# Optimization experiments

Hardware: AMD Instinct MI355X
Metric: run time of the kernel (lower is better)

The kernel has to match this reference:

```python
import jax, jax.numpy as jnp
import numpy as np

N = 20000      # nodes per snapshot
E = 320000     # directed edges per snapshot (self-loops added in reference)
T = 8          # snapshot sequence length
IN = 1         # in_dim
H = 32         # hidden_dim
HEADS = 2      # heads in first GAT layer
EPS = 1e-16    # PyG softmax denominator epsilon


def setup_inputs() -> dict:
    key = jax.random.key(0)
    ks = jax.random.split(key, 20)
    s = 0.1  # weight scale for numerical sanity
    return {
        "x": jax.random.normal(ks[0], (T, N, IN), jnp.float32),
        "edge_index": jax.random.randint(ks[1], (T, 2, E), 0, N, jnp.int64),
        # GAT layer 1: in=1 -> heads=2, out=32 (concat -> 64)
        "W1": jax.random.normal(ks[2], (IN, HEADS * H), jnp.float32) * s,
        "att_src1": jax.random.normal(ks[3], (HEADS, H), jnp.float32) * s,
        "att_dst1": jax.random.normal(ks[4], (HEADS, H), jnp.float32) * s,
        "b1": jax.random.normal(ks[5], (HEADS * H,), jnp.float32) * s,
        # GAT layer 2: in=64 -> heads=1, out=32
        "W2": jax.random.normal(ks[6], (HEADS * H, H), jnp.float32) * s,
        "att_src2": jax.random.normal(ks[7], (1, H), jnp.float32) * s,
        "att_dst2": jax.random.normal(ks[8], (1, H), jnp.float32) * s,
        "b2": jax.random.normal(ks[9], (H,), jnp.float32) * s,
        # GRU (torch layout: rows ordered r,z,n)
        "gru_w_ih": jax.random.normal(ks[10], (3 * H, H), jnp.float32) * s,
        "gru_w_hh": jax.random.normal(ks[11], (3 * H, H), jnp.float32) * s,
        "gru_b_ih": jax.random.normal(ks[12], (3 * H,), jnp.float32) * s,
        "gru_b_hh": jax.random.normal(ks[13], (3 * H,), jnp.float32) * s,
        # output head
        "fc_w": jax.random.normal(ks[14], (1, H), jnp.float32) * s,
        "fc_b": jax.random.normal(ks[15], (1,), jnp.float32) * s,
    }


def _gat_layer(x, src, dst, W, att_src, att_dst, bias, heads, dh):
    """PyG GATConv (shared src/dst lin, leaky_relu 0.2, per-dest softmax, concat heads)."""
    h = (x @ W).reshape(N, heads, dh)                      # [N,Hd,D]
    a_src = jnp.sum(h * att_src, axis=-1)                  # [N,Hd]
    a_dst = jnp.sum(h * att_dst, axis=-1)                  # [N,Hd]
    e = jax.nn.leaky_relu(a_src[src] + a_dst[dst], 0.2)    # [Eh,Hd]
    m = jax.ops.segment_max(e, dst, num_segments=N)        # per-dest max (stable)
    ex = jnp.exp(e - m[dst])
    denom = jax.ops.segment_sum(ex, dst, num_segments=N)
    alpha = ex / (denom[dst] + EPS)                        # [Eh,Hd]
    msg = h[src] * alpha[..., None]                        # [Eh,Hd,D]
    out = jax.ops.segment_sum(msg, dst, num_segments=N)    # [N,Hd,D]
    return out.reshape(N, heads * dh) + bias


def _encode(x_t, ei_t, W1, att_src1, att_dst1, b1, W2, att_src2, att_dst2, b2):
    loops = jnp.arange(N, dtype=ei_t.dtype)                # GATConv add_self_loops=True
    src = jnp.concatenate([ei_t[0], loops])
    dst = jnp.concatenate([ei_t[1], loops])
    h = jax.nn.elu(_gat_layer(x_t, src, dst, W1, att_src1, att_dst1, b1, HEADS, H))
    h = jax.nn.elu(_gat_layer(h, src, dst, W2, att_src2, att_dst2, b2, 1, H))
    return h                                                # [N,H]


def reference(x, edge_index, W1, att_src1, att_dst1, b1, W2, att_src2, att_dst2, b2,
              gru_w_ih, gru_w_hh, gru_b_ih, gru_b_hh, fc_w, fc_b):
    enc = jax.vmap(lambda xt, et: _encode(xt, et, W1, att_src1, att_dst1, b1,
                                          W2, att_src2, att_dst2, b2))(x, edge_index)  # [T,N,H]

    def gru_step(h, x_t):
        gi = x_t @ gru_w_ih.T + gru_b_ih                   # [N,3H]
        gh = h @ gru_w_hh.T + gru_b_hh
        ir, iz, in_ = jnp.split(gi, 3, axis=-1)
        hr, hz, hn = jnp.split(gh, 3, axis=-1)
        r = jax.nn.sigmoid(ir + hr)
        z = jax.nn.sigmoid(iz + hz)
        n = jnp.tanh(in_ + r * hn)
        h_new = (1.0 - z) * n + z * h
        return h_new, None

    h0 = jnp.zeros((N, H), enc.dtype)
    h_last, _ = jax.lax.scan(gru_step, h0, enc)            # last timestep hidden [N,H]
    pred = h_last @ fc_w.T + fc_b                          # [N,1]
    return pred
```

## Files before the change

kernel.cpp:

```cpp
#include <hip/hip_runtime.h>
#include <cmath>

#define NN 20000
#define NE 320000
#define TT 8
#define EPSF 1e-16f
#define NR 32
#define RSZ 625
#define NCH 1250

#define OFF_RT  0
#define OFF_ROW 1024
#define OFF_CSR (OFF_ROW + TT*(NN+1))
#define OFF_H2S (OFF_CSR + TT*NE/2)
#define OFF_AS2 (OFF_H2S + TT*NN*32)
#define OFF_AD2 (OFF_AS2 + TT*NN)
#define OFF_ENC (OFF_AD2 + TT*NN)
#define OFF_WP  (OFF_ENC + TT*NN*32)
#define WS_WORDS (OFF_WP + 6144)

__device__ __forceinline__ float fexp(float x) { return __expf(x); }
__device__ __forceinline__ float fsigmoid(float x) { return 1.f / (1.f + __expf(-x)); }
__device__ __forceinline__ float ftanh(float x) {
    float ax = fabsf(x);
    float e2 = __expf(-2.f * ax);
    float th = (1.f - e2) / (1.f + e2);
    return copysignf(th, x);
}

__global__ __launch_bounds__(256) void k_bhist(const int* __restrict__ ei,
                                               int* __restrict__ bh,
                                               const float* __restrict__ wih,
                                               const float* __restrict__ whh,
                                               float* __restrict__ wp) {
    int b = blockIdx.x;
    int t = b & 7, c = b >> 3;
    __shared__ int cnt[NR];
    int tid = threadIdx.x;
    if (b < 4) {
        int i = b * 256 + tid;
        int k = i >> 5, j = i & 31;
        ((float4*)wp)[i] = make_float4(wih[j * 32 + k], wih[(32 + j) * 32 + k],
                                       wih[(64 + j) * 32 + k], whh[j * 32 + k]);
        ((float2*)(wp + 4096))[i] = make_float2(whh[(32 + j) * 32 + k],
                                                whh[(64 + j) * 32 + k]);
    }
    if (tid < NR) cnt[tid] = 0;
    __syncthreads();
    int e = c * 256 + tid;
    int dst = ei[(size_t)t * 2 * NE + NE + e];
    int r = dst / RSZ;
    atomicAdd(&cnt[r], 1);
    __syncthreads();
    if (tid < NR) bh[(t * NCH + c) * NR + tid] = cnt[tid];
}

__global__ __launch_bounds__(256) void k_bscan1(int* __restrict__ bh,
                                                int* __restrict__ rt) {
    int b = blockIdx.x;
    int t = b & 7, r = b >> 3;
    __shared__ int sums[256];
    int tid = threadIdx.x;
    int c0 = tid * 5, c1 = c0 + 5; if (c1 > NCH) c1 = NCH; if (c0 > NCH) c0 = NCH;
    int v[5]; int s = 0;
    for (int c = c0, k = 0; c < c1; c++, k++) { v[k] = bh[(t * NCH + c) * NR + r]; s += v[k]; }
    sums[tid] = s;
    __syncthreads();
    if (tid == 0) {
        int acc = 0;
        for (int i = 0; i < 256; i++) { int x = sums[i]; sums[i] = acc; acc += x; }
        rt[t * NR + r] = acc;
    }
    __syncthreads();
    int acc = sums[tid];
    for (int c = c0, k = 0; c < c1; c++, k++) { bh[(t * NCH + c) * NR + r] = acc; acc += v[k]; }
}

__global__ __launch_bounds__(256) void k_bplace(const int* __restrict__ ei,
                                                const int* __restrict__ bh,
                                                const int* __restrict__ rt,
                                                unsigned* __restrict__ bkt) {
    int b = blockIdx.x;
    int t = b & 7, c = b >> 3;
    __shared__ int cnt[NR], base[NR], rbs[NR];
    int tid = threadIdx.x;
    if (tid == 0) {
        int acc = 0;
        for (int r = 0; r < NR; r++) { rbs[r] = acc; acc += rt[t * NR + r]; }
    }
    if (tid < NR) {
        cnt[tid] = 0;
        base[tid] = bh[(t * NCH + c) * NR + tid];
    }
    __syncthreads();
    int e = c * 256 + tid;
    int src = ei[(size_t)t * 2 * NE + e];
    int dst = ei[(size_t)t * 2 * NE + NE + e];
    int r = dst / RSZ;
    int pos = atomicAdd(&cnt[r], 1);
    bkt[(size_t)t * NE + rbs[r] + base[r] + pos] =
        ((unsigned)src << 10) | (unsigned)(dst - r * RSZ);
}

__global__ __launch_bounds__(256) void k_csr(const unsigned* __restrict__ bkt,
                                             const int* __restrict__ rt,
                                             int* __restrict__ row,
                                             unsigned short* __restrict__ csr) {
    int b = blockIdx.x;
    int t = b & 7, r = b >> 3;
    __shared__ int segs[2];
    __shared__ int deg[RSZ];
    __shared__ int cur[RSZ];
    __shared__ int sums[256];
    int tid = threadIdx.x;
    if (tid == 0) {
        int acc = 0, s0 = 0;
        for (int i = 0; i < NR; i++) { if (i == r) s0 = acc; acc += rt[t * NR + i]; }
        segs[0] = s0;
        segs[1] = (r == NR - 1) ? acc : s0 + rt[t * NR + r];
    }
    for (int i = tid; i < RSZ; i += 256) deg[i] = 0;
    __syncthreads();
    int seg0 = segs[0], seg1 = segs[1];
    int lo = r * RSZ;
    const unsigned* bp = bkt + (size_t)t * NE;
    for (int i = seg0 + tid; i < seg1; i += 256)
        atomicAdd(&deg[bp[i] & 1023], 1);
    __syncthreads();
    int c0 = tid * 3, c1 = c0 + 3; if (c1 > RSZ) c1 = RSZ; if (c0 > RSZ) c0 = RSZ;
    int v[3]; int s = 0;
    for (int i = c0, k = 0; i < c1; i++, k++) { v[k] = deg[i]; s += v[k]; }
    sums[tid] = s;
    __syncthreads();
    if (tid == 0) {
        int acc = 0;
        for (int i = 0; i < 256; i++) { int x = sums[i]; sums[i] = acc; acc += x; }
    }
    __syncthreads();
    int acc = sums[tid];
    for (int i = c0, k = 0; i < c1; i++, k++) {
        int off = seg0 + acc;
        row[t * (NN + 1) + lo + i] = off;
        cur[i] = off;
        acc += v[k];
    }
    if (r == NR - 1 && tid == 0) row[t * (NN + 1) + NN] = seg1;
    __syncthreads();
    unsigned short* cp = csr + (size_t)t * NE;
    for (int i = seg0 + tid; i < seg1; i += 256) {
        unsigned pk = bp[i];
        int pos = atomicAdd(&cur[pk & 1023], 1);
        cp[pos] = (unsigned short)(pk >> 10);
    }
}

__global__ __launch_bounds__(256) void k_l1(
        const float* __restrict__ x, const int* __restrict__ row,
        const unsigned short* __restrict__ csr,
        const float* __restrict__ as1, const float* __restrict__ ad1,
        const float* __restrict__ W1, const float* __restrict__ b1,
        const float* __restrict__ W2,
        const float* __restrict__ as2w, const float* __restrict__ ad2w,
        float* __restrict__ h2s, float* __restrict__ as2, float* __restrict__ ad2) {
    __shared__ float sW2[64 * 32];
    __shared__ float sW1[64], sb1[64], sas[32], sad[32], sc[4];
    int tid = threadIdx.x;
    for (int i = tid; i < 64 * 32; i += 256) sW2[i] = W2[i];
    if (tid < 64) { sW1[tid] = W1[tid]; sb1[tid] = b1[tid]; }
    if (tid < 32) { sas[tid] = as2w[tid]; sad[tid] = ad2w[tid]; }
    if (tid < 4) {
        int hd = tid & 1;
        const float* att = (tid < 2) ? as1 : ad1;
        float s = 0.f;
        for (int k = 0; k < 32; k++) s += W1[hd * 32 + k] * att[hd * 32 + k];
        sc[tid] = s;
    }
    __syncthreads();
    int b = blockIdx.x;
    int t = b & 7, chunk = b >> 3;
    int n = chunk * 256 + tid;
    if (n >= NN) return;
    int idx = t * NN + n;
    float cs0 = sc[0], cs1 = sc[1], cd0 = sc[2], cd1 = sc[3];
    float xd = x[idx];
    float v0 = xd * (cs0 + cd0); v0 = v0 > 0.f ? v0 : 0.2f * v0; float ex0 = fexp(v0);
    float v1 = xd * (cs1 + cd1); v1 = v1 > 0.f ? v1 : 0.2f * v1; float ex1 = fexp(v1);
    float den0 = ex0, den1 = ex1, S0 = ex0 * xd, S1 = ex1 * xd;
    int rs = row[t * (NN + 1) + n], re = row[t * (NN + 1) + n + 1];
    const unsigned short* cp = csr + (size_t)t * NE;
    const float* xp = x + t * NN;
    int i = rs;
    for (; i < re && (i & 3); i++) {
        int src = cp[i];
        float xs = xp[src];
        float u0 = xs * cs0 + xd * cd0; u0 = u0 > 0.f ? u0 : 0.2f * u0; float q0 = fexp(u0);
        float u1 = xs * cs1 + xd * cd1; u1 = u1 > 0.f ? u1 : 0.2f * u1; float q1 = fexp(u1);
        den0 += q0; S0 += q0 * xs;
        den1 += q1; S1 += q1 * xs;
    }
    for (; i + 4 <= re; i += 4) {
        ushort4 s4 = *(const ushort4*)(cp + i);
        float xA = xp[s4.x], xB = xp[s4.y], xC = xp[s4.z], xD = xp[s4.w];
        float uA0 = xA * cs0 + xd * cd0; uA0 = uA0 > 0.f ? uA0 : 0.2f * uA0; float qA0 = fexp(uA0);
        float uB0 = xB * cs0 + xd * cd0; uB0 = uB0 > 0.f ? uB0 : 0.2f * uB0; float qB0 = fexp(uB0);
        float uC0 = xC * cs0 + xd * cd0; uC0 = uC0 > 0.f ? uC0 : 0.2f * uC0; float qC0 = fexp(uC0);
        float uD0 = xD * cs0 + xd * cd0; uD0 = uD0 > 0.f ? uD0 : 0.2f * uD0; float qD0 = fexp(uD0);
        float uA1 = xA * cs1 + xd * cd1; uA1 = uA1 > 0.f ? uA1 : 0.2f * uA1; float qA1 = fexp(uA1);
        float uB1 = xB * cs1 + xd * cd1; uB1 = uB1 > 0.f ? uB1 : 0.2f * uB1; float qB1 = fexp(uB1);
        float uC1 = xC * cs1 + xd * cd1; uC1 = uC1 > 0.f ? uC1 : 0.2f * uC1; float qC1 = fexp(uC1);
        float uD1 = xD * cs1 + xd * cd1; uD1 = uD1 > 0.f ? uD1 : 0.2f * uD1; float qD1 = fexp(uD1);
        den0 += (qA0 + qB0) + (qC0 + qD0);
        S0 += qA0 * xA + qB0 * xB + qC0 * xC + qD0 * xD;
        den1 += (qA1 + qB1) + (qC1 + qD1);
        S1 += qA1 * xA + qB1 * xB + qC1 * xC + qD1 * xD;
    }
    for (; i < re; i++) {
        int src = cp[i];
        float xs = xp[src];
        float u0 = xs * cs0 + xd * cd0; u0 = u0 > 0.f ? u0 : 0.2f * u0; float q0 = fexp(u0);
        float u1 = xs * cs1 + xd * cd1; u1 = u1 > 0.f ? u1 : 0.2f * u1; float q1 = fexp(u1);
        den0 += q0; S0 += q0 * xs;
        den1 += q1; S1 += q1 * xs;
    }
    S0 /= (den0 + EPSF);
    S1 /= (den1 + EPSF);
    float h1[64];
#pragma unroll
    for (int d = 0; d < 64; d++) {
        float v = sW1[d] * (d < 32 ? S0 : S1) + sb1[d];
        h1[d] = v > 0.f ? v : fexp(v) - 1.f;
    }
    float a_s = 0.f, a_d = 0.f;
    float acc[32];
#pragma unroll 4
    for (int j = 0; j < 32; j++) {
        float a = 0.f;
#pragma unroll
        for (int d = 0; d < 64; d++) a += h1[d] * sW2[d * 32 + j];
        acc[j] = a;
        a_s += a * sas[j];
        a_d += a * sad[j];
    }
    float4* op = (float4*)(h2s + (size_t)idx * 32);
#pragma unroll
    for (int q = 0; q < 8; q++)
        op[q] = make_float4(acc[4 * q], acc[4 * q + 1], acc[4 * q + 2], acc[4 * q + 3]);
    as2[idx] = a_s;
    ad2[idx] = a_d;
}

__global__ __launch_bounds__(256) void k_l2(
        const int* __restrict__ row, const unsigned short* __restrict__ csr,
        const float* __restrict__ as2, const float* __restrict__ ad2,
        const float* __restrict__ h2s, const float* __restrict__ b2,
        float* __restrict__ enc) {
    __shared__ float2 qoff[8][32];
    int tid = threadIdx.x;
    int g = tid >> 5, lane = tid & 31;
    int b = blockIdx.x;
    int t = b & 7, chunk = b >> 3;
    int n = chunk * 8 + g;
    int pair = t * NN + n;
    int base = t * NN;
    const float* hb = h2s + (size_t)base * 32;
    float adn = ad2[pair];
    float vs = as2[pair] + adn; vs = vs > 0.f ? vs : 0.2f * vs;
    float qs = fexp(vs);
    float num = qs * hb[(size_t)n * 32 + lane];
    float den_part = 0.f;
    int rs = row[t * (NN + 1) + n], re = row[t * (NN + 1) + n + 1];
    const unsigned short* cp = csr + (size_t)t * NE;
    for (int i0 = rs; i0 < re; i0 += 32) {
        int cnt = re - i0; if (cnt > 32) cnt = 32;
        float q = 0.f;
        if (lane < cnt) {
            int s = cp[i0 + lane];
            float a = as2[base + s];
            float u = a + adn; u = u > 0.f ? u : 0.2f * u;
            q = fexp(u);
            qoff[g][lane] = make_float2(q, __int_as_float(s * 32));
        }
        den_part += q;
        __builtin_amdgcn_wave_barrier();
        int e = 0;
        for (; e + 4 <= cnt; e += 4) {
            float4 p0 = *(const float4*)&qoff[g][e];
            float4 p1 = *(const float4*)&qoff[g][e + 2];
            num += p0.x * hb[__float_as_int(p0.y) + lane];
            num += p0.z * hb[__float_as_int(p0.w) + lane];
            num += p1.x * hb[__float_as_int(p1.y) + lane];
            num += p1.z * hb[__float_as_int(p1.w) + lane];
        }
        for (; e + 2 <= cnt; e += 2) {
            float4 p0 = *(const float4*)&qoff[g][e];
            num += p0.x * hb[__float_as_int(p0.y) + lane];
            num += p0.z * hb[__float_as_int(p0.w) + lane];
        }
        if (e < cnt) {
            float2 p = qoff[g][e];
            num += p.x * hb[__float_as_int(p.y) + lane];
        }
        __builtin_amdgcn_wave_barrier();
    }
    float den = den_part;
#pragma unroll
    for (int off = 16; off > 0; off >>= 1) den += __shfl_xor(den, off, 32);
    den += qs;
    float ev = num / (den + EPSF) + b2[lane];
    ev = ev > 0.f ? ev : fexp(ev) - 1.f;
    enc[(size_t)pair * 32 + lane] = ev;
}

__global__ __launch_bounds__(128) void k_gru(
        const float* __restrict__ enc, const float* __restrict__ wp,
        const float* __restrict__ bih, const float* __restrict__ bhh,
        const float* __restrict__ fcw, const float* __restrict__ fcb,
        float* __restrict__ out) {
    __shared__ float4 wpA[32 * 32];
    __shared__ float2 wpB[32 * 32];
    __shared__ float sbih[96], sbhh[96], sfw[32];
    __shared__ float4 e4[4][32], h4[4][32];
    int tid = threadIdx.x;
    const float4* wpAg = (const float4*)wp;
    const float2* wpBg = (const float2*)(wp + 4096);
    for (int i = tid; i < 1024; i += 128) { wpA[i] = wpAg[i]; wpB[i] = wpBg[i]; }
    if (tid < 96) { sbih[tid] = bih[tid]; sbhh[tid] = bhh[tid]; }
    if (tid < 32) sfw[tid] = fcw[tid];
    int g = tid >> 5, lane = tid & 31;
    int n0 = blockIdx.x * 16 + g * 4;
    float h0 = 0.f, h1 = 0.f, h2 = 0.f, h3 = 0.f;
    h4[g][lane] = make_float4(0.f, 0.f, 0.f, 0.f);
    __syncthreads();
    float bi_r = sbih[lane], bi_z = sbih[32 + lane], bi_n = sbih[64 + lane];
    float bh_r = sbhh[lane], bh_z = sbhh[32 + lane], bh_n = sbhh[64 + lane];
    const float* ep0 = enc + (size_t)n0 * 32 + lane;
    float4 ecur = make_float4(ep0[0], ep0[32], ep0[64], ep0[96]);
    for (int t = 0; t < TT; t++) {
        e4[g][lane] = ecur;
        __builtin_amdgcn_wave_barrier();
        if (t < TT - 1) {
            const float* ep = enc + ((size_t)((t + 1) * NN + n0)) * 32 + lane;
            ecur = make_float4(ep[0], ep[32], ep[64], ep[96]);
        }
        float ir0 = bi_r, ir1 = bi_r, ir2 = bi_r, ir3 = bi_r;
        float iz0 = bi_z, iz1 = bi_z, iz2 = bi_z, iz3 = bi_z;
        float in0 = bi_n, in1 = bi_n, in2 = bi_n, in3 = bi_n;
        float hr0 = bh_r, hr1 = bh_r, hr2 = bh_r, hr3 = bh_r;
        float hz0 = bh_z, hz1 = bh_z, hz2 = bh_z, hz3 = bh_z;
        float hn0 = bh_n, hn1 = bh_n, hn2 = bh_n, hn3 = bh_n;
#pragma unroll 16
        for (int k = 0; k < 32; k++) {
            float4 wa = wpA[k * 32 + lane];
            float2 wb = wpB[k * 32 + lane];
            float4 ek = e4[g][k];
            float4 hk = h4[g][k];
            ir0 += wa.x * ek.x; ir1 += wa.x * ek.y; ir2 += wa.x * ek.z; ir3 += wa.x * ek.w;
            iz0 += wa.y * ek.x; iz1 += wa.y * ek.y; iz2 += wa.y * ek.z; iz3 += wa.y * ek.w;
            in0 += wa.z * ek.x; in1 += wa.z * ek.y; in2 += wa.z * ek.z; in3 += wa.z * ek.w;
            hr0 += wa.w * hk.x; hr1 += wa.w * hk.y; hr2 += wa.w * hk.z; hr3 += wa.w * hk.w;
            hz0 += wb.x * hk.x; hz1 += wb.x * hk.y; hz2 += wb.x * hk.z; hz3 += wb.x * hk.w;
            hn0 += wb.y * hk.x; hn1 += wb.y * hk.y; hn2 += wb.y * hk.z; hn3 += wb.y * hk.w;
        }
        __builtin_amdgcn_wave_barrier();
        {
            float r, z, nn_;
            r = fsigmoid(ir0 + hr0); z = fsigmoid(iz0 + hz0);
            nn_ = ftanh(in0 + r * hn0); h0 = (1.f - z) * nn_ + z * h0;
            r = fsigmoid(ir1 + hr1); z = fsigmoid(iz1 + hz1);
            nn_ = ftanh(in1 + r * hn1); h1 = (1.f - z) * nn_ + z * h1;
            r = fsigmoid(ir2 + hr2); z = fsigmoid(iz2 + hz2);
            nn_ = ftanh(in2 + r * hn2); h2 = (1.f - z) * nn_ + z * h2;
            r = fsigmoid(ir3 + hr3); z = fsigmoid(iz3 + hz3);
            nn_ = ftanh(in3 + r * hn3); h3 = (1.f - z) * nn_ + z * h3;
        }
        h4[g][lane] = make_float4(h0, h1, h2, h3);
        __builtin_amdgcn_wave_barrier();
    }
    float fw = sfw[lane], fb = fcb[0];
    float v0 = h0 * fw, v1 = h1 * fw, v2 = h2 * fw, v3 = h3 * fw;
#pragma unroll
    for (int off = 16; off > 0; off >>= 1) {
        v0 += __shfl_down(v0, off, 32);
        v1 += __shfl_down(v1, off, 32);
        v2 += __shfl_down(v2, off, 32);
        v3 += __shfl_down(v3, off, 32);
    }
    if (lane == 0) {
        out[n0 + 0] = v0 + fb;
        out[n0 + 1] = v1 + fb;
        out[n0 + 2] = v2 + fb;
        out[n0 + 3] = v3 + fb;
    }
}

extern "C" void kernel_launch(void* const* d_in, const int* in_sizes, int n_in,
                              void* d_out, int out_size, void* d_ws, size_t ws_size,
                              hipStream_t stream) {
    const float* x    = (const float*)d_in[0];
    const int*   ei   = (const int*)d_in[1];
    const float* W1   = (const float*)d_in[2];
    const float* as1  = (const float*)d_in[3];
    const float* ad1  = (const float*)d_in[4];
    const float* b1   = (const float*)d_in[5];
    const float* W2   = (const float*)d_in[6];
    const float* as2w = (const float*)d_in[7];
    const float* ad2w = (const float*)d_in[8];
    const float* b2   = (const float*)d_in[9];
    const float* wih  = (const float*)d_in[10];
    const float* whh  = (const float*)d_in[11];
    const float* bih  = (const float*)d_in[12];
    const float* bhh  = (const float*)d_in[13];
    const float* fcw  = (const float*)d_in[14];
    const float* fcb  = (const float*)d_in[15];
    float* ws  = (float*)d_ws;
    float* out = (float*)d_out;

    int*            rt   = (int*)(ws + OFF_RT);
    int*            rowp = (int*)(ws + OFF_ROW);
    unsigned short* csr  = (unsigned short*)(ws + OFF_CSR);
    int*            bh   = (int*)(ws + OFF_H2S);
    unsigned*       bkt  = (unsigned*)(ws + OFF_ENC);
    float*          wp   = ws + OFF_WP;

    k_bhist<<<TT * NCH, 256, 0, stream>>>(ei, bh, wih, whh, wp);
    k_bscan1<<<TT * NR, 256, 0, stream>>>(bh, rt);
    k_bplace<<<TT * NCH, 256, 0, stream>>>(ei, bh, rt, bkt);
    k_csr<<<TT * NR, 256, 0, stream>>>(bkt, rt, rowp, csr);

    k_l1<<<TT * ((NN + 255) / 256), 256, 0, stream>>>(x, rowp, csr, as1, ad1,
                                              W1, b1, W2, as2w, ad2w,
                                              ws + OFF_H2S, ws + OFF_AS2, ws + OFF_AD2);

    k_l2<<<TT * (NN / 8), 256, 0, stream>>>(rowp, csr, ws + OFF_AS2, ws + OFF_AD2,
                                            ws + OFF_H2S, b2, ws + OFF_ENC);

    k_gru<<<NN / 16, 128, 0, stream>>>(ws + OFF_ENC, wp, bih, bhh,
                                       fcw, fcb, out);
}
```

Measured before the change: 256.4 us.

## Precompute GRU input projections for all timesteps before recurrent loop

The GRU kernel now computes the input-gate projections for all 8 timesteps in a first loop, keeping them in registers (48 floats per thread), then runs the recurrence with only the hidden-state matvec on the serial path. Each wave handles 2 nodes instead of 4 with 256-thread blocks, and the packed weight layout is split into separate input and hidden arrays. This shortens the dependent chain per step and adds waves, at the cost of higher register pressure from the stored projections.

```diff
diff --git a/kernel.cpp b/kernel.cpp
--- a/kernel.cpp
+++ b/kernel.cpp
@@ -40,10 +40,10 @@
     if (b < 4) {
         int i = b * 256 + tid;
         int k = i >> 5, j = i & 31;
-        ((float4*)wp)[i] = make_float4(wih[j * 32 + k], wih[(32 + j) * 32 + k],
-                                       wih[(64 + j) * 32 + k], whh[j * 32 + k]);
-        ((float2*)(wp + 4096))[i] = make_float2(whh[(32 + j) * 32 + k],
-                                                whh[(64 + j) * 32 + k]);
+        ((float2*)wp)[i] = make_float2(wih[j * 32 + k], wih[(32 + j) * 32 + k]);
+        wp[2048 + i] = wih[(64 + j) * 32 + k];
+        ((float2*)(wp + 3072))[i] = make_float2(whh[j * 32 + k], whh[(32 + j) * 32 + k]);
+        wp[5120 + i] = whh[(64 + j) * 32 + k];
     }
     if (tid < NR) cnt[tid] = 0;
     __syncthreads();
@@ -311,85 +311,94 @@
     enc[(size_t)pair * 32 + lane] = ev;
 }
 
-__global__ __launch_bounds__(128) void k_gru(
+__global__ __launch_bounds__(256) void k_gru(
         const float* __restrict__ enc, const float* __restrict__ wp,
         const float* __restrict__ bih, const float* __restrict__ bhh,
         const float* __restrict__ fcw, const float* __restrict__ fcb,
         float* __restrict__ out) {
-    __shared__ float4 wpA[32 * 32];
-    __shared__ float2 wpB[32 * 32];
+    __shared__ float2 wIa[1024];
+    __shared__ float  wIb[1024];
+    __shared__ float2 wHa[1024];
+    __shared__ float  wHb[1024];
     __shared__ float sbih[96], sbhh[96], sfw[32];
-    __shared__ float4 e4[4][32], h4[4][32];
-    int tid = threadIdx.x;
-    const float4* wpAg = (const float4*)wp;
-    const float2* wpBg = (const float2*)(wp + 4096);
-    for (int i = tid; i < 1024; i += 128) { wpA[i] = wpAg[i]; wpB[i] = wpBg[i]; }
+    __shared__ float2 ebuf[8][32], hbuf[8][32];
+    int tid = threadIdx.x;
+    for (int i = tid; i < 1024; i += 256) {
+        wIa[i] = ((const float2*)wp)[i];
+        wIb[i] = wp[2048 + i];
+        wHa[i] = ((const float2*)(wp + 3072))[i];
+        wHb[i] = wp[5120 + i];
+    }
     if (tid < 96) { sbih[tid] = bih[tid]; sbhh[tid] = bhh[tid]; }
     if (tid < 32) sfw[tid] = fcw[tid];
     int g = tid >> 5, lane = tid & 31;
-    int n0 = blockIdx.x * 16 + g * 4;
-    float h0 = 0.f, h1 = 0.f, h2 = 0.f, h3 = 0.f;
-    h4[g][lane] = make_float4(0.f, 0.f, 0.f, 0.f);
-    __syncthreads();
+    int n0 = blockIdx.x * 16 + g * 2;
+    float h0 = 0.f, h1 = 0.f;
+    hbuf[g][lane] = make_float2(0.f, 0.f);
+    __syncthreads();
+    float gi[TT][6];
+#pragma unroll
+    for (int t = 0; t < TT; t++)
+#pragma unroll
+        for (int q = 0; q < 6; q++) gi[t][q] = 0.f;
+    const float* ebase = enc + (size_t)n0 * 32 + lane;
+    float e0 = ebase[0], e1 = ebase[32];
+#pragma unroll
+    for (int t = 0; t < TT; t++) {
+        ebuf[g][lane] = make_float2(e0, e1);
+        __builtin_amdgcn_wave_barrier();
+        if (t < TT - 1) {
+            const float* ep = ebase + (size_t)(t + 1) * NN * 32;
+            e0 = ep[0]; e1 = ep[32];
+        }
+#pragma unroll
+        for (int k = 0; k < 32; k++) {
+            float2 wa = wIa[k * 32 + lane];
+            float  wn = wIb[k * 32 + lane];
+            float2 ek = ebuf[g][k];
+            gi[t][0] += wa.x * ek.x; gi[t][1] += wa.x * ek.y;
+            gi[t][2] += wa.y * ek.x; gi[t][3] += wa.y * ek.y;
+            gi[t][4] += wn   * ek.x; gi[t][5] += wn   * ek.y;
+        }
+        __builtin_amdgcn_wave_barrier();
+    }
     float bi_r = sbih[lane], bi_z = sbih[32 + lane], bi_n = sbih[64 + lane];
     float bh_r = sbhh[lane], bh_z = sbhh[32 + lane], bh_n = sbhh[64 + lane];
-    const float* ep0 = enc + (size_t)n0 * 32 + lane;
-    float4 ecur = make_float4(ep0[0], ep0[32], ep0[64], ep0[96]);
+#pragma unroll
     for (int t = 0; t < TT; t++) {
-        e4[g][lane] = ecur;
-        __builtin_amdgcn_wave_barrier();
-        if (t < TT - 1) {
-            const float* ep = enc + ((size_t)((t + 1) * NN + n0)) * 32 + lane;
-            ecur = make_float4(ep[0], ep[32], ep[64], ep[96]);
-        }
-        float ir0 = bi_r, ir1 = bi_r, ir2 = bi_r, ir3 = bi_r;
-        float iz0 = bi_z, iz1 = bi_z, iz2 = bi_z, iz3 = bi_z;
-        float in0 = bi_n, in1 = bi_n, in2 = bi_n, in3 = bi_n;
-        float hr0 = bh_r, hr1 = bh_r, hr2 = bh_r, hr3 = bh_r;
-        float hz0 = bh_z, hz1 = bh_z, hz2 = bh_z, hz3 = bh_z;
-        float hn0 = bh_n, hn1 = bh_n, hn2 = bh_n, hn3 = bh_n;
-#pragma unroll 16
+        float hr0 = bh_r, hr1 = bh_r, hz0 = bh_z, hz1 = bh_z;
+        float hn0 = bh_n, hn1 = bh_n;
+#pragma unroll
         for (int k = 0; k < 32; k++) {
-            float4 wa = wpA[k * 32 + lane];
-            float2 wb = wpB[k * 32 + lane];
-            float4 ek = e4[g][k];
-            float4 hk = h4[g][k];
-            ir0 += wa.x * ek.x; ir1 += wa.x * ek.y; ir2 += wa.x * ek.z; ir3 += wa.x * ek.w;
-            iz0 += wa.y * ek.x; iz1 += wa.y * ek.y; iz2 += wa.y * ek.z; iz3 += wa.y * ek.w;
-            in0 += wa.z * ek.x; in1 += wa.z * ek.y; in2 += wa.z * ek.z; in3 += wa.z * ek.w;
-            hr0 += wa.w * hk.x; hr1 += wa.w * hk.y; hr2 += wa.w * hk.z; hr3 += wa.w * hk.w;
-            hz0 += wb.x * hk.x; hz1 += wb.x * hk.y; hz2 += wb.x * hk.z; hz3 += wb.x * hk.w;
-            hn0 += wb.y * hk.x; hn1 += wb.y * hk.y; hn2 += wb.y * hk.z; hn3 += wb.y * hk.w;
-        }
-        __builtin_amdgcn_wave_barrier();
-        {
-            float r, z, nn_;
-            r = fsigmoid(ir0 + hr0); z = fsigmoid(iz0 + hz0);
-            nn_ = ftanh(in0 + r * hn0); h0 = (1.f - z) * nn_ + z * h0;
-            r = fsigmoid(ir1 + hr1); z = fsigmoid(iz1 + hz1);
-            nn_ = ftanh(in1 + r * hn1); h1 = (1.f - z) * nn_ + z * h1;
-            r = fsigmoid(ir2 + hr2); z = fsigmoid(iz2 + hz2);
-            nn_ = ftanh(in2 + r * hn2); h2 = (1.f - z) * nn_ + z * h2;
-            r = fsigmoid(ir3 + hr3); z = fsigmoid(iz3 + hz3);
-            nn_ = ftanh(in3 + r * hn3); h3 = (1.f - z) * nn_ + z * h3;
-        }
-        h4[g][lane] = make_float4(h0, h1, h2, h3);
+            float2 wa = wHa[k * 32 + lane];
+            float  wn = wHb[k * 32 + lane];
+            float2 hk = hbuf[g][k];
+            hr0 += wa.x * hk.x; hr1 += wa.x * hk.y;
+            hz0 += wa.y * hk.x; hz1 += wa.y * hk.y;
+            hn0 += wn   * hk.x; hn1 += wn   * hk.y;
+        }
+        __builtin_amdgcn_wave_barrier();
+        float r0 = fsigmoid(gi[t][0] + bi_r + hr0);
+        float r1 = fsigmoid(gi[t][1] + bi_r + hr1);
+        float z0 = fsigmoid(gi[t][2] + bi_z + hz0);
+        float z1 = fsigmoid(gi[t][3] + bi_z + hz1);
+        float nn0 = ftanh(gi[t][4] + bi_n + r0 * hn0);
+        float nn1 = ftanh(gi[t][5] + bi_n + r1 * hn1);
+        h0 = (1.f - z0) * nn0 + z0 * h0;
+        h1 = (1.f - z1) * nn1 + z1 * h1;
+        hbuf[g][lane] = make_float2(h0, h1);
         __builtin_amdgcn_wave_barrier();
     }
     float fw = sfw[lane], fb = fcb[0];
-    float v0 = h0 * fw, v1 = h1 * fw, v2 = h2 * fw, v3 = h3 * fw;
+    float v0 = h0 * fw, v1 = h1 * fw;
 #pragma unroll
     for (int off = 16; off > 0; off >>= 1) {
         v0 += __shfl_down(v0, off, 32);
         v1 += __shfl_down(v1, off, 32);
-        v2 += __shfl_down(v2, off, 32);
-        v3 += __shfl_down(v3, off, 32);
     }
     if (lane == 0) {
         out[n0 + 0] = v0 + fb;
         out[n0 + 1] = v1 + fb;
-        out[n0 + 2] = v2 + fb;
-        out[n0 + 3] = v3 + fb;
     }
 }
 
@@ -434,6 +443,6 @@
     k_l2<<<TT * (NN / 8), 256, 0, stream>>>(rowp, csr, ws + OFF_AS2, ws + OFF_AD2,
                                             ws + OFF_H2S, b2, ws + OFF_ENC);
 
-    k_gru<<<NN / 16, 128, 0, stream>>>(ws + OFF_ENC, wp, bih, bhh,
+    k_gru<<<NN / 16, 256, 0, stream>>>(ws + OFF_ENC, wp, bih, bhh,
                                        fcw, fcb, out);
 }
```

New measurement: 303.6 us. 18.4% more time.
